# Performance work log

Hardware: AMD Instinct MI355X
Metric: run time of the kernel (lower is better)

## Reference

```python
import jax, jax.numpy as jnp
import numpy as np

EMB = 1024
HEADS = 8
HEAD_DIM = EMB // HEADS


def setup_inputs() -> dict:
    key = jax.random.key(0)
    ks = jax.random.split(key, 11)
    B, S = 4, 2048
    scale = 1.0 / np.sqrt(EMB)
    inp = {
        "query": jax.random.normal(ks[0], (B, S, EMB), jnp.float32),
        "key": jax.random.normal(ks[1], (B, S, EMB), jnp.float32),
        "value": jax.random.normal(ks[2], (B, S, EMB), jnp.float32),
        "Wq": jax.random.normal(ks[3], (EMB, EMB), jnp.float32) * scale,
        "bq": jnp.zeros((EMB,), jnp.float32),
        "Wk": jax.random.normal(ks[4], (EMB, EMB), jnp.float32) * scale,
        "bk": jnp.zeros((EMB,), jnp.float32),
        "Wv": jax.random.normal(ks[5], (EMB, EMB), jnp.float32) * scale,
        "bv": jnp.zeros((EMB,), jnp.float32),
        "Wo": jax.random.normal(ks[6], (EMB, EMB), jnp.float32) * scale,
        "bo": jnp.zeros((EMB,), jnp.float32),
    }
    return inp


def _split_heads(x):
    B, S, _ = x.shape
    return x.reshape(B, S, HEADS, HEAD_DIM).transpose(0, 2, 1, 3)  # [B,H,S,D]


def reference(query, key, value, Wq, bq, Wk, bk, Wv, bv, Wo, bo):
    Q = _split_heads(query @ Wq.T + bq)
    K = _split_heads(key @ Wk.T + bk)
    V = _split_heads(value @ Wv.T + bv)
    # [B,H,S,S] attention scores, scaled by sqrt(head_dim)
    scores = jnp.einsum("bhqd,bhkd->bhqk", Q, K) / jnp.sqrt(
        jnp.asarray(HEAD_DIM, Q.dtype)
    )
    attention = jax.nn.softmax(scores, axis=-1)
    # dropout is identity in eval mode
    x = jnp.einsum("bhqk,bhkd->bhqd", attention, V)
    B, H, S, D = x.shape
    x = x.transpose(0, 2, 1, 3).reshape(B, S, EMB)
    x = x @ Wo.T + bo
    return (x, attention)
```

## Files before the change

### kernel.cpp

```cpp
#include <hip/hip_runtime.h>
#include <hip/hip_bf16.h>
#include <math.h>

#define BB 4
#define SS 2048
#define EMB 1024
#define HH 8
#define DD 128

typedef __attribute__((ext_vector_type(8))) short bf16x8;
typedef __attribute__((ext_vector_type(4))) float f32x4;

__device__ __forceinline__ unsigned short f2bf(float f) {
    unsigned u = __builtin_bit_cast(unsigned, f);
    u += 0x7FFFu + ((u >> 16) & 1u);
    return (unsigned short)(u >> 16);
}

__device__ __forceinline__ void gload_lds16(const void* g, void* l) {
    __builtin_amdgcn_global_load_lds(
        (const __attribute__((address_space(1))) unsigned int*)g,
        (__attribute__((address_space(3))) unsigned int*)l, 16, 0, 0);
}

#define SB0 __builtin_amdgcn_sched_barrier(0)

__global__ void f2bf3_kernel(const float* __restrict__ a, const float* __restrict__ b,
                             const float* __restrict__ c, unsigned short* __restrict__ dst,
                             int n4) {
    const float* src = blockIdx.z == 0 ? a : (blockIdx.z == 1 ? b : c);
    unsigned short* d = dst + (size_t)blockIdx.z * ((size_t)n4 * 4);
    int i = blockIdx.x * blockDim.x + threadIdx.x;
    int stride = gridDim.x * blockDim.x;
    for (; i < n4; i += stride) {
        float4 f = ((const float4*)src)[i];
        ushort4 o;
        o.x = f2bf(f.x); o.y = f2bf(f.y); o.z = f2bf(f.z); o.w = f2bf(f.w);
        ((ushort4*)d)[i] = o;
    }
}

__global__ void f2bf4_kernel(const float* __restrict__ a, const float* __restrict__ b,
                             const float* __restrict__ c, const float* __restrict__ e,
                             unsigned short* __restrict__ dst, int n4) {
    const float* src = blockIdx.z == 0 ? a : (blockIdx.z == 1 ? b : (blockIdx.z == 2 ? c : e));
    unsigned short* d = dst + (size_t)blockIdx.z * ((size_t)n4 * 4);
    int i = blockIdx.x * blockDim.x + threadIdx.x;
    int stride = gridDim.x * blockDim.x;
    for (; i < n4; i += stride) {
        float4 f = ((const float4*)src)[i];
        ushort4 o;
        o.x = f2bf(f.x); o.y = f2bf(f.y); o.z = f2bf(f.z); o.w = f2bf(f.w);
        ((ushort4*)d)[i] = o;
    }
}

template <int MODE>
__device__ __forceinline__ void gemm_core(const unsigned short* __restrict__ A,
                                          const unsigned short* __restrict__ Bw,
                                          const float* __restrict__ bias,
                                          void* __restrict__ Cout, float scale)
{
    __shared__ short As[2][128 * 32];
    __shared__ short Bs[2][128 * 32];
    const int K = 1024;
    const int m0 = blockIdx.x * 128, n0 = blockIdx.y * 128;
    const int t = threadIdx.x;
    const int lane = t & 63, w = t >> 6;
    const int wr = w >> 1, wc = w & 1;
    const int g = lane >> 4, li = lane & 15;
    f32x4 acc[4][4] = {};

    auto stage = [&](int k0, int buf) {
        #pragma unroll
        for (int i = 0; i < 2; ++i) {
            int idx = i * 256 + t;
            int row = idx >> 2, col = (idx & 3) * 8;
            gload_lds16(A  + (size_t)(m0 + row) * K + k0 + col, &As[buf][idx * 8]);
            gload_lds16(Bw + (size_t)(n0 + row) * K + k0 + col, &Bs[buf][idx * 8]);
        }
    };

    stage(0, 0);
    for (int ki = 0; ki < 32; ++ki) {
        const int cur = ki & 1;
        if (ki < 31) {
            stage((ki + 1) * 32, cur ^ 1);
            asm volatile("s_waitcnt vmcnt(4)" ::: "memory");
        } else {
            asm volatile("s_waitcnt vmcnt(0)" ::: "memory");
        }
        SB0; __builtin_amdgcn_s_barrier(); SB0;

        bf16x8 af[4], bfr[4];
        #pragma unroll
        for (int mi = 0; mi < 4; ++mi)
            af[mi] = *(const bf16x8*)&As[cur][(wr * 64 + mi * 16 + li) * 32 + g * 8];
        #pragma unroll
        for (int ni = 0; ni < 4; ++ni)
            bfr[ni] = *(const bf16x8*)&Bs[cur][(wc * 64 + ni * 16 + li) * 32 + g * 8];
        #pragma unroll
        for (int mi = 0; mi < 4; ++mi) {
            #pragma unroll
            for (int ni = 0; ni < 4; ++ni)
                acc[mi][ni] = __builtin_amdgcn_mfma_f32_16x16x32_bf16(
                    af[mi], bfr[ni], acc[mi][ni], 0, 0, 0);
        }
        asm volatile("s_waitcnt lgkmcnt(0)" ::: "memory");
        SB0; __builtin_amdgcn_s_barrier(); SB0;
    }

    #pragma unroll
    for (int mi = 0; mi < 4; ++mi) {
        #pragma unroll
        for (int ni = 0; ni < 4; ++ni) {
            int n = n0 + wc * 64 + ni * 16 + li;
            float bv = bias[n];
            #pragma unroll
            for (int i = 0; i < 4; ++i) {
                int m = m0 + wr * 64 + mi * 16 + g * 4 + i;
                float v = acc[mi][ni][i] + bv;
                if (MODE == 0) {
                    v *= scale;
                    int b = m >> 11, s = m & 2047, h = n >> 7, d = n & 127;
                    ((unsigned short*)Cout)[((((size_t)b * HH + h) * SS + s) << 7) + d] = f2bf(v);
                } else {
                    ((float*)Cout)[(size_t)m * EMB + n] = v;
                }
            }
        }
    }
}

__global__ __launch_bounds__(256, 2)
void gemm_qkv(const unsigned short* __restrict__ XB, const unsigned short* __restrict__ WB,
              const float* __restrict__ bq, const float* __restrict__ bk,
              const float* __restrict__ bv, unsigned short* __restrict__ QKVb, float qscale)
{
    const size_t NX = (size_t)BB * SS * EMB;
    const size_t NW = (size_t)EMB * EMB;
    const int z = blockIdx.z;
    const float* bias = z == 0 ? bq : (z == 1 ? bk : bv);
    gemm_core<0>(XB + z * NX, WB + z * NW, bias, QKVb + z * NX, z == 0 ? qscale : 1.f);
}

__global__ __launch_bounds__(256, 2)
void gemm_out(const unsigned short* __restrict__ Ob, const unsigned short* __restrict__ Wo,
              const float* __restrict__ bo, float* __restrict__ outx)
{
    gemm_core<1>(Ob, Wo, bo, outx, 1.f);
}

__global__ __launch_bounds__(256, 2)
void attn_kernel(const unsigned short* __restrict__ Qb,
                 const unsigned short* __restrict__ Kb,
                 const unsigned short* __restrict__ Vb,
                 float* __restrict__ attn,
                 unsigned short* __restrict__ Ob)
{
    __shared__ short Ks[64 * 128];
    __shared__ short Vt[128 * 64];
    __shared__ short Ps[4][16 * 68];

    const int t = threadIdx.x;
    const int lane = t & 63, w = t >> 6;
    const int g = lane >> 4, li = lane & 15;
    const int bh = blockIdx.y;
    const int q0 = blockIdx.x * 64 + w * 16;

    const unsigned short* Kbh = Kb + (size_t)bh * SS * DD;
    const unsigned short* Vbh = Vb + (size_t)bh * SS * DD;

    bf16x8 qf[4];
    {
        const unsigned short* qp = Qb + ((size_t)bh * SS + q0 + li) * DD + g * 8;
        #pragma unroll
        for (int kk = 0; kk < 4; ++kk) qf[kk] = *(const bf16x8*)(qp + kk * 32);
    }

    float lacc[4] = {0.f, 0.f, 0.f, 0.f};

    auto stageK = [&](int kt2, char* dst) {
        const char* ksrc = (const char*)(Kbh + kt2 * 64 * DD);
        #pragma unroll
        for (int i = 0; i < 4; ++i) {
            int lb = (i * 256 + t) * 16;
            int row = lb >> 8;
            gload_lds16(ksrc + (lb ^ ((row & 7) << 4)), dst + lb);
        }
    };

    stageK(0, (char*)Ks);
    for (int kt = 0; kt < 32; ++kt) {
        const char* cur = (kt & 1) ? (const char*)Vt : (const char*)Ks;
        char* nxt = (kt & 1) ? (char*)Ks : (char*)Vt;
        if (kt < 31) {
            stageK(kt + 1, nxt);
            asm volatile("s_waitcnt vmcnt(4)" ::: "memory");
        } else {
            asm volatile("s_waitcnt vmcnt(0)" ::: "memory");
        }
        SB0; __builtin_amdgcn_s_barrier(); SB0;

        #pragma unroll
        for (int kc = 0; kc < 4; ++kc) {
            f32x4 a = {0.f, 0.f, 0.f, 0.f};
            int row = kc * 16 + li;
            int sw = (row & 7) << 4;
            #pragma unroll
            for (int kk = 0; kk < 4; ++kk) {
                bf16x8 kf = *(const bf16x8*)(cur + row * 256 + ((kk * 64 + g * 16) ^ sw));
                a = __builtin_amdgcn_mfma_f32_16x16x32_bf16(qf[kk], kf, a, 0, 0, 0);
            }
            #pragma unroll
            for (int i = 0; i < 4; ++i)
                lacc[i] += __builtin_amdgcn_exp2f(a[i]);
        }
        __builtin_amdgcn_s_barrier(); SB0;
    }

    float rl[4];
    #pragma unroll
    for (int i = 0; i < 4; ++i) {
        float ts = lacc[i];
        #pragma unroll
        for (int mk = 1; mk < 16; mk <<= 1) ts += __shfl_xor(ts, mk, 64);
        rl[i] = 1.f / ts;
    }

    f32x4 O[8] = {};
    float* arow = attn + (size_t)bh * SS * SS;

    bf16x8 va[2], vbr[2];
    #pragma unroll
    for (int i = 0; i < 2; ++i) {
        int idx = i * 256 + t;
        int k0 = (idx >> 4) * 2, d0 = (idx & 15) * 8;
        va[i]  = *(const bf16x8*)(Vbh + k0 * DD + d0);
        vbr[i] = *(const bf16x8*)(Vbh + (k0 + 1) * DD + d0);
    }

    for (int kt = 0; kt < 32; ++kt) {
        __syncthreads();
        const char* ksrc = (const char*)(Kbh + kt * 64 * DD);
        #pragma unroll
        for (int i = 0; i < 4; ++i) {
            int lb = (i * 256 + t) * 16;
            int row = lb >> 8;
            gload_lds16(ksrc + (lb ^ ((row & 7) << 4)), (char*)Ks + lb);
        }
        #pragma unroll
        for (int i = 0; i < 2; ++i) {
            int idx = i * 256 + t;
            int kpair = idx >> 4, d0 = (idx & 15) * 8;
            #pragma unroll
            for (int j = 0; j < 8; ++j) {
                unsigned pk = (unsigned)(unsigned short)va[i][j]
                            | ((unsigned)(unsigned short)vbr[i][j] << 16);
                int d = d0 + j;
                int ba = (d * 128 + kpair * 4) ^ (((d ^ (d >> 3)) & 7) << 4);
                *(unsigned*)((char*)Vt + ba) = pk;
            }
        }
        __syncthreads();

        if (kt < 31) {
            const unsigned short* vn = Vbh + (kt + 1) * 64 * DD;
            #pragma unroll
            for (int i = 0; i < 2; ++i) {
                int idx = i * 256 + t;
                int k0 = (idx >> 4) * 2, d0 = (idx & 15) * 8;
                va[i]  = *(const bf16x8*)(vn + k0 * DD + d0);
                vbr[i] = *(const bf16x8*)(vn + (k0 + 1) * DD + d0);
            }
        }

        #pragma unroll
        for (int kc = 0; kc < 4; ++kc) {
            f32x4 a = {0.f, 0.f, 0.f, 0.f};
            int row = kc * 16 + li;
            int sw = (row & 7) << 4;
            #pragma unroll
            for (int kk = 0; kk < 4; ++kk) {
                bf16x8 kf = *(const bf16x8*)((const char*)Ks + row * 256 + ((kk * 64 + g * 16) ^ sw));
                a = __builtin_amdgcn_mfma_f32_16x16x32_bf16(qf[kk], kf, a, 0, 0, 0);
            }
            #pragma unroll
            for (int i = 0; i < 4; ++i) {
                float p = __builtin_amdgcn_exp2f(a[i]) * rl[i];
                int qr = g * 4 + i;
                __builtin_nontemporal_store(p, &arow[(size_t)(q0 + qr) * SS + kt * 64 + kc * 16 + li]);
                Ps[w][qr * 68 + kc * 16 + li] = (short)f2bf(p);
            }
        }
        asm volatile("s_waitcnt lgkmcnt(0)" ::: "memory");
        SB0;

        bf16x8 pf0 = *(const bf16x8*)&Ps[w][li * 68 + g * 8];
        bf16x8 pf1 = *(const bf16x8*)&Ps[w][li * 68 + 32 + g * 8];
        #pragma unroll
        for (int dt = 0; dt < 8; ++dt) {
            int dr = dt * 16 + li;
            int vsw = ((dr ^ (dr >> 3)) & 7) << 4;
            bf16x8 vf0 = *(const bf16x8*)((const char*)Vt + dr * 128 + ((g * 16) ^ vsw));
            bf16x8 vf1 = *(const bf16x8*)((const char*)Vt + dr * 128 + ((64 + g * 16) ^ vsw));
            O[dt] = __builtin_amdgcn_mfma_f32_16x16x32_bf16(pf0, vf0, O[dt], 0, 0, 0);
            O[dt] = __builtin_amdgcn_mfma_f32_16x16x32_bf16(pf1, vf1, O[dt], 0, 0, 0);
        }
    }

    const int b = bh >> 3, h = bh & 7;
    #pragma unroll
    for (int dt = 0; dt < 8; ++dt) {
        #pragma unroll
        for (int i = 0; i < 4; ++i) {
            size_t r = (size_t)b * SS + q0 + g * 4 + i;
            Ob[r * EMB + h * DD + dt * 16 + li] = f2bf(O[dt][i]);
        }
    }
}

extern "C" void kernel_launch(void* const* d_in, const int* in_sizes, int n_in,
                              void* d_out, int out_size, void* d_ws, size_t ws_size,
                              hipStream_t stream)
{
    const float* q  = (const float*)d_in[0];
    const float* k  = (const float*)d_in[1];
    const float* v  = (const float*)d_in[2];
    const float* Wq = (const float*)d_in[3];
    const float* bq = (const float*)d_in[4];
    const float* Wk = (const float*)d_in[5];
    const float* bk = (const float*)d_in[6];
    const float* Wv = (const float*)d_in[7];
    const float* bv = (const float*)d_in[8];
    const float* Wo = (const float*)d_in[9];
    const float* bo = (const float*)d_in[10];

    const size_t NX = (size_t)BB * SS * EMB;
    const size_t NW = (size_t)EMB * EMB;

    unsigned short* Qb = (unsigned short*)d_ws;
    unsigned short* Ob = Qb + 3 * NX;
    unsigned short* WB = Ob + NX;

    float* outx = (float*)d_out;
    float* attn = outx + NX;
    unsigned short* XB = (unsigned short*)attn;

    f2bf3_kernel<<<dim3(1024, 1, 3), 256, 0, stream>>>(q, k, v, XB, (int)(NX / 4));
    f2bf4_kernel<<<dim3(128, 1, 4), 256, 0, stream>>>(Wq, Wk, Wv, Wo, WB, (int)(NW / 4));

    const float qscale = 1.4426950408889634f / sqrtf((float)DD);
    gemm_qkv<<<dim3(64, 8, 3), 256, 0, stream>>>(XB, WB, bq, bk, bv, Qb, qscale);

    attn_kernel<<<dim3(32, 32), 256, 0, stream>>>(Qb, Qb + NX, Qb + 2 * NX, attn, Ob);

    gemm_out<<<dim3(64, 8), 256, 0, stream>>>(Ob, WB + 3 * NW, bo, outx);
}
```

Measured before the change: 359.6 us.

## Emit V transposed from QKV GEMM and read K/V directly from global in attention

The V projection epilogue now writes V in a transposed [B,H,D,S] layout, so the attention kernel can load V^T fragments straight from global memory instead of transposing V through LDS. K tiles are likewise loaded directly into registers per wave rather than staged through shared memory with async loads and barriers. This removes the LDS staging, the in-kernel transpose and most block-level synchronization. In exchange each wave issues its own redundant global loads and loses the prefetch overlap, and the transposed V store from the GEMM epilogue is strided and poorly coalesced.

```diff
diff --git a/kernel.cpp b/kernel.cpp
--- a/kernel.cpp
+++ b/kernel.cpp
@@ -124,6 +124,9 @@
                     v *= scale;
                     int b = m >> 11, s = m & 2047, h = n >> 7, d = n & 127;
                     ((unsigned short*)Cout)[((((size_t)b * HH + h) * SS + s) << 7) + d] = f2bf(v);
+                } else if (MODE == 2) {
+                    int b = m >> 11, s = m & 2047, h = n >> 7, d = n & 127;
+                    ((unsigned short*)Cout)[(((size_t)b * HH + h) * DD + d) * SS + s] = f2bf(v);
                 } else {
                     ((float*)Cout)[(size_t)m * EMB + n] = v;
                 }
@@ -140,8 +143,9 @@
     const size_t NX = (size_t)BB * SS * EMB;
     const size_t NW = (size_t)EMB * EMB;
     const int z = blockIdx.z;
-    const float* bias = z == 0 ? bq : (z == 1 ? bk : bv);
-    gemm_core<0>(XB + z * NX, WB + z * NW, bias, QKVb + z * NX, z == 0 ? qscale : 1.f);
+    if (z == 0)      gemm_core<0>(XB,          WB,          bq, QKVb,          qscale);
+    else if (z == 1) gemm_core<0>(XB + NX,     WB + NW,     bk, QKVb + NX,     1.f);
+    else             gemm_core<2>(XB + 2 * NX, WB + 2 * NW, bv, QKVb + 2 * NX, 1.f);
 }
 
 __global__ __launch_bounds__(256, 2)
@@ -154,12 +158,10 @@
 __global__ __launch_bounds__(256, 2)
 void attn_kernel(const unsigned short* __restrict__ Qb,
                  const unsigned short* __restrict__ Kb,
-                 const unsigned short* __restrict__ Vb,
+                 const unsigned short* __restrict__ VTb,
                  float* __restrict__ attn,
                  unsigned short* __restrict__ Ob)
 {
-    __shared__ short Ks[64 * 128];
-    __shared__ short Vt[128 * 64];
     __shared__ short Ps[4][16 * 68];
 
     const int t = threadIdx.x;
@@ -168,8 +170,8 @@
     const int bh = blockIdx.y;
     const int q0 = blockIdx.x * 64 + w * 16;
 
-    const unsigned short* Kbh = Kb + (size_t)bh * SS * DD;
-    const unsigned short* Vbh = Vb + (size_t)bh * SS * DD;
+    const unsigned short* Kbh  = Kb  + (size_t)bh * SS * DD;
+    const unsigned short* VTbh = VTb + (size_t)bh * SS * DD;
 
     bf16x8 qf[4];
     {
@@ -180,43 +182,24 @@
 
     float lacc[4] = {0.f, 0.f, 0.f, 0.f};
 
-    auto stageK = [&](int kt2, char* dst) {
-        const char* ksrc = (const char*)(Kbh + kt2 * 64 * DD);
-        #pragma unroll
-        for (int i = 0; i < 4; ++i) {
-            int lb = (i * 256 + t) * 16;
-            int row = lb >> 8;
-            gload_lds16(ksrc + (lb ^ ((row & 7) << 4)), dst + lb);
-        }
-    };
-
-    stageK(0, (char*)Ks);
     for (int kt = 0; kt < 32; ++kt) {
-        const char* cur = (kt & 1) ? (const char*)Vt : (const char*)Ks;
-        char* nxt = (kt & 1) ? (char*)Ks : (char*)Vt;
-        if (kt < 31) {
-            stageK(kt + 1, nxt);
-            asm volatile("s_waitcnt vmcnt(4)" ::: "memory");
-        } else {
-            asm volatile("s_waitcnt vmcnt(0)" ::: "memory");
-        }
-        SB0; __builtin_amdgcn_s_barrier(); SB0;
-
+        const unsigned short* kbase = Kbh + kt * 64 * DD;
+        bf16x8 kf[16];
+        #pragma unroll
+        for (int kc = 0; kc < 4; ++kc)
+            #pragma unroll
+            for (int kk = 0; kk < 4; ++kk)
+                kf[kc * 4 + kk] = *(const bf16x8*)(kbase + (kc * 16 + li) * DD + kk * 32 + g * 8);
         #pragma unroll
         for (int kc = 0; kc < 4; ++kc) {
             f32x4 a = {0.f, 0.f, 0.f, 0.f};
-            int row = kc * 16 + li;
-            int sw = (row & 7) << 4;
-            #pragma unroll
-            for (int kk = 0; kk < 4; ++kk) {
-                bf16x8 kf = *(const bf16x8*)(cur + row * 256 + ((kk * 64 + g * 16) ^ sw));
-                a = __builtin_amdgcn_mfma_f32_16x16x32_bf16(qf[kk], kf, a, 0, 0, 0);
-            }
+            #pragma unroll
+            for (int kk = 0; kk < 4; ++kk)
+                a = __builtin_amdgcn_mfma_f32_16x16x32_bf16(qf[kk], kf[kc * 4 + kk], a, 0, 0, 0);
             #pragma unroll
             for (int i = 0; i < 4; ++i)
                 lacc[i] += __builtin_amdgcn_exp2f(a[i]);
         }
-        __builtin_amdgcn_s_barrier(); SB0;
     }
 
     float rl[4];
@@ -231,60 +214,20 @@
     f32x4 O[8] = {};
     float* arow = attn + (size_t)bh * SS * SS;
 
-    bf16x8 va[2], vbr[2];
-    #pragma unroll
-    for (int i = 0; i < 2; ++i) {
-        int idx = i * 256 + t;
-        int k0 = (idx >> 4) * 2, d0 = (idx & 15) * 8;
-        va[i]  = *(const bf16x8*)(Vbh + k0 * DD + d0);
-        vbr[i] = *(const bf16x8*)(Vbh + (k0 + 1) * DD + d0);
-    }
-
     for (int kt = 0; kt < 32; ++kt) {
-        __syncthreads();
-        const char* ksrc = (const char*)(Kbh + kt * 64 * DD);
-        #pragma unroll
-        for (int i = 0; i < 4; ++i) {
-            int lb = (i * 256 + t) * 16;
-            int row = lb >> 8;
-            gload_lds16(ksrc + (lb ^ ((row & 7) << 4)), (char*)Ks + lb);
-        }
-        #pragma unroll
-        for (int i = 0; i < 2; ++i) {
-            int idx = i * 256 + t;
-            int kpair = idx >> 4, d0 = (idx & 15) * 8;
-            #pragma unroll
-            for (int j = 0; j < 8; ++j) {
-                unsigned pk = (unsigned)(unsigned short)va[i][j]
-                            | ((unsigned)(unsigned short)vbr[i][j] << 16);
-                int d = d0 + j;
-                int ba = (d * 128 + kpair * 4) ^ (((d ^ (d >> 3)) & 7) << 4);
-                *(unsigned*)((char*)Vt + ba) = pk;
-            }
-        }
-        __syncthreads();
-
-        if (kt < 31) {
-            const unsigned short* vn = Vbh + (kt + 1) * 64 * DD;
-            #pragma unroll
-            for (int i = 0; i < 2; ++i) {
-                int idx = i * 256 + t;
-                int k0 = (idx >> 4) * 2, d0 = (idx & 15) * 8;
-                va[i]  = *(const bf16x8*)(vn + k0 * DD + d0);
-                vbr[i] = *(const bf16x8*)(vn + (k0 + 1) * DD + d0);
-            }
-        }
-
+        const unsigned short* kbase = Kbh + kt * 64 * DD;
+        bf16x8 kf[16];
+        #pragma unroll
+        for (int kc = 0; kc < 4; ++kc)
+            #pragma unroll
+            for (int kk = 0; kk < 4; ++kk)
+                kf[kc * 4 + kk] = *(const bf16x8*)(kbase + (kc * 16 + li) * DD + kk * 32 + g * 8);
         #pragma unroll
         for (int kc = 0; kc < 4; ++kc) {
             f32x4 a = {0.f, 0.f, 0.f, 0.f};
-            int row = kc * 16 + li;
-            int sw = (row & 7) << 4;
-            #pragma unroll
-            for (int kk = 0; kk < 4; ++kk) {
-                bf16x8 kf = *(const bf16x8*)((const char*)Ks + row * 256 + ((kk * 64 + g * 16) ^ sw));
-                a = __builtin_amdgcn_mfma_f32_16x16x32_bf16(qf[kk], kf, a, 0, 0, 0);
-            }
+            #pragma unroll
+            for (int kk = 0; kk < 4; ++kk)
+                a = __builtin_amdgcn_mfma_f32_16x16x32_bf16(qf[kk], kf[kc * 4 + kk], a, 0, 0, 0);
             #pragma unroll
             for (int i = 0; i < 4; ++i) {
                 float p = __builtin_amdgcn_exp2f(a[i]) * rl[i];
@@ -298,12 +241,12 @@
 
         bf16x8 pf0 = *(const bf16x8*)&Ps[w][li * 68 + g * 8];
         bf16x8 pf1 = *(const bf16x8*)&Ps[w][li * 68 + 32 + g * 8];
+
         #pragma unroll
         for (int dt = 0; dt < 8; ++dt) {
-            int dr = dt * 16 + li;
-            int vsw = ((dr ^ (dr >> 3)) & 7) << 4;
-            bf16x8 vf0 = *(const bf16x8*)((const char*)Vt + dr * 128 + ((g * 16) ^ vsw));
-            bf16x8 vf1 = *(const bf16x8*)((const char*)Vt + dr * 128 + ((64 + g * 16) ^ vsw));
+            const unsigned short* vrow = VTbh + (size_t)(dt * 16 + li) * SS + kt * 64 + g * 8;
+            bf16x8 vf0 = *(const bf16x8*)(vrow);
+            bf16x8 vf1 = *(const bf16x8*)(vrow + 32);
             O[dt] = __builtin_amdgcn_mfma_f32_16x16x32_bf16(pf0, vf0, O[dt], 0, 0, 0);
             O[dt] = __builtin_amdgcn_mfma_f32_16x16x32_bf16(pf1, vf1, O[dt], 0, 0, 0);
         }
```

Result: slower. 828.7 us (+130.5%).
